# Performance work log

Measured on AMD Instinct MI355X. Metric: run time of the kernel, lower is better.

Reference implementation:

```python
import jax, jax.numpy as jnp
import numpy as np

B, S, D = 1, 2048, 1024          # batch, seq, n_embd
E, F = 16, 1024                  # n_routed_experts, moe_intermediate_size
NG, TKG, K = 4, 2, 4             # n_group, topk_group, num_experts_per_tok
NSH = 2                          # n_shared_experts
SCALE = 2.5                      # routed_scaling_factor
STD = 0.02
EPG = E // NG                    # experts per group


def setup_inputs() -> dict:
    key = jax.random.key(0)
    ks = jax.random.split(key, 8)
    return {
        "hidden_states": jax.random.normal(ks[0], (B, S, D), jnp.float32),
        "router_w": jax.random.normal(ks[1], (E, D), jnp.float32) * STD,   # gate.weight
        "bias": jnp.zeros((E,), jnp.float32),                              # e_score_correction_bias
        "gate_w": jax.random.normal(ks[2], (E, D, F), jnp.float32) * STD,  # per-expert gate_proj (transposed)
        "up_w": jax.random.normal(ks[3], (E, D, F), jnp.float32) * STD,    # per-expert up_proj
        "down_w": jax.random.normal(ks[4], (E, F, D), jnp.float32) * STD,  # per-expert down_proj
        "sh_gate_w": jax.random.normal(ks[5], (D, NSH * F), jnp.float32) * STD,
        "sh_up_w": jax.random.normal(ks[6], (D, NSH * F), jnp.float32) * STD,
        "sh_down_w": jax.random.normal(ks[7], (NSH * F, D), jnp.float32) * STD,
    }


def _route(x_flat, router_w, bias):
    # x_flat: [T, D] -> topk_idx [T, K], topk_w [T, K]
    logits = x_flat.astype(jnp.float32) @ router_w.T          # [T, E]
    scores = jax.nn.sigmoid(logits)
    s = scores + bias[None, :]                                # scores_for_choice
    sg = s.reshape(-1, NG, EPG)
    group_score = jax.lax.top_k(sg, 2)[0].sum(-1)             # sum of top-2 per group [T, NG]
    gidx = jax.lax.top_k(group_score, TKG)[1]                 # [T, TKG]
    gmask = jnp.sum(jax.nn.one_hot(gidx, NG, dtype=jnp.float32), axis=1) > 0   # [T, NG]
    emask = jnp.repeat(gmask, EPG, axis=1)                    # [T, E]
    masked = jnp.where(emask, s, -1.0)
    topk_idx = jax.lax.top_k(masked, K)[1]                    # [T, K]
    tw = jnp.take_along_axis(scores, topk_idx, axis=1)        # gather raw sigmoid scores
    tw = tw / (tw.sum(-1, keepdims=True) + 1e-20)             # norm_topk_prob
    tw = tw * SCALE
    return topk_idx, tw


def reference(hidden_states, router_w, bias, gate_w, up_w, down_w,
              sh_gate_w, sh_up_w, sh_down_w):
    x = hidden_states.reshape(-1, D)                          # [T, D]
    topk_idx, tw = _route(x, router_w, bias)
    # combine weights per (token, expert): scatter-add of topk weights
    combine = (jax.nn.one_hot(topk_idx, E, dtype=tw.dtype) * tw[..., None]).sum(1)  # [T, E]
    # per-expert SwiGLU MLPs (dense dispatch, masked combine == index_add semantics)
    h = jnp.einsum('td,edf->etf', x, gate_w)                  # [E, T, F]
    u = jnp.einsum('td,edf->etf', x, up_w)
    y = jnp.einsum('etf,efd->etd', jax.nn.silu(h) * u, down_w)  # [E, T, D]
    routed = jnp.einsum('etd,te->td', y, combine)             # weighted combine
    # shared experts
    sh = (jax.nn.silu(x @ sh_gate_w) * (x @ sh_up_w)) @ sh_down_w
    return (routed + sh).reshape(hidden_states.shape)
```

## Files before the change

### kernel.cpp

```cpp
#include <hip/hip_runtime.h>
#include <cstdint>
#include <cstddef>


#define T_TOK 2048
#define DIM   1024
#define NEXP  16
#define MAXTILES 80
#define SH_TILES 32
#define GRID_Y (MAXTILES + SH_TILES)
#define NBLK (8 * GRID_Y)
#define ABASE_SH 10240

typedef __bf16 bf16x8_t __attribute__((ext_vector_type(8)));
typedef float  f32x4_t  __attribute__((ext_vector_type(4)));
typedef unsigned short ushort8_t __attribute__((ext_vector_type(8)));
typedef unsigned short ushort4_t __attribute__((ext_vector_type(4)));

#define OFF_XB     (0UL)
#define OFF_SHGT   (4UL<<20)
#define OFF_SHUT   (8UL<<20)
#define OFF_GATET  (12UL<<20)
#define OFF_UPT    (44UL<<20)
#define OFF_DOWNT  (76UL<<20)
#define OFF_SHDT   (108UL<<20)
#define OFF_ACT    (112UL<<20)
#define OFF_YSLOT  (140UL<<20)
#define OFF_PART   (0UL)
#define OFF_CTRL   (160UL<<20)
#define CT_OFFSETS  128
#define CT_NTILES   192
#define CT_TILEEXP  256
#define CT_SLOTTOK  4096
#define CT_TKSLOT   49152
#define CT_TOPKIDX  81920
#define CT_TOPKW    114688

__device__ __forceinline__ unsigned short f2bf(float f) {
  __bf16 h = (__bf16)f;
  return __builtin_bit_cast(unsigned short, h);
}
__device__ __forceinline__ float bf2f(unsigned short u) {
  unsigned int v = ((unsigned int)u) << 16;
  return __builtin_bit_cast(float, v);
}
__device__ __forceinline__ void gld16(const void* g, void* l) {
  __builtin_amdgcn_global_load_lds(
      (const __attribute__((address_space(1))) void*)(g),
      (__attribute__((address_space(3))) void*)(l), 16, 0, 0);
}

__device__ __forceinline__ void tbody(const float* __restrict__ src,
                                      unsigned short* __restrict__ dst,
                                      int R, int C) {
  __shared__ unsigned short tile[64 * 68];
  int cT = blockIdx.x * 64, rT = blockIdx.y * 64;
  int t = threadIdx.x;
  int rb = t >> 4, cb = t & 15;
  float f[4][4];
#pragma unroll
  for (int i = 0; i < 4; i++) {
    float4 v = *(const float4*)(src + (long)(rT + 4 * rb + i) * C + cT + 4 * cb);
    f[i][0] = v.x; f[i][1] = v.y; f[i][2] = v.z; f[i][3] = v.w;
  }
#pragma unroll
  for (int j = 0; j < 4; j++) {
    ushort4_t o;
    o[0] = f2bf(f[0][j]); o[1] = f2bf(f[1][j]); o[2] = f2bf(f[2][j]); o[3] = f2bf(f[3][j]);
    int c = 4 * cb + j;
    *(ushort4_t*)&tile[c * 68 + 4 * rb] = o;
  }
  __syncthreads();
#pragma unroll
  for (int p = 0; p < 2; p++) {
    int q = t + 256 * p;
    int c = q >> 3, r0 = (q & 7) * 8;
    ushort4_t lo = *(const ushort4_t*)&tile[c * 68 + r0];
    ushort4_t hi = *(const ushort4_t*)&tile[c * 68 + r0 + 4];
    ushort8_t w8 = {lo[0], lo[1], lo[2], lo[3], hi[0], hi[1], hi[2], hi[3]};
    *(ushort8_t*)(dst + (long)(cT + c) * R + rT + r0) = w8;
  }
}

__global__ void k_transpose(const float* __restrict__ src, unsigned short* __restrict__ dst,
                            int R, int C) {
  long b = blockIdx.z;
  tbody(src + b * (long)R * C, dst + b * (long)R * C, R, C);
}

__global__ void k_transpose3(const float* __restrict__ g, const float* __restrict__ u,
                             const float* __restrict__ d, unsigned short* __restrict__ gT,
                             unsigned short* __restrict__ uT, unsigned short* __restrict__ dT) {
  int z = blockIdx.z;
  int which = z >> 4;
  long b = z & 15;
  const float* s = (which == 0) ? g : (which == 1) ? u : d;
  unsigned short* t = (which == 0) ? gT : (which == 1) ? uT : dT;
  tbody(s + b * 1048576L, t + b * 1048576L, 1024, 1024);
}

__global__ void k_transpose_sh(const float* __restrict__ sg, const float* __restrict__ su,
                               unsigned short* __restrict__ gT, unsigned short* __restrict__ uT) {
  const float* s = blockIdx.z ? su : sg;
  unsigned short* t = blockIdx.z ? uT : gT;
  tbody(s, t, 1024, 2048);
}

__global__ __launch_bounds__(256) void k_router(
    const float* __restrict__ x, const float* __restrict__ rw,
    const float* __restrict__ bias, int* __restrict__ topk_idx,
    float* __restrict__ topk_w, unsigned short* __restrict__ xb) {
  int t = blockIdx.x, tid = threadIdx.x;
  int wv = tid >> 6, lane = tid & 63;
  float4 xv = ((const float4*)(x + (size_t)t * DIM))[tid];
  ushort4_t xo;
  xo[0] = f2bf(xv.x); xo[1] = f2bf(xv.y); xo[2] = f2bf(xv.z); xo[3] = f2bf(xv.w);
  ((ushort4_t*)(xb + (size_t)t * DIM))[tid] = xo;
  float part[NEXP];
#pragma unroll
  for (int e = 0; e < NEXP; e++) {
    float4 wr = ((const float4*)(rw + (size_t)e * DIM))[tid];
    part[e] = xv.x * wr.x + xv.y * wr.y + xv.z * wr.z + xv.w * wr.w;
  }
  __shared__ float wsum_s[4 * NEXP];
#pragma unroll
  for (int e = 0; e < NEXP; e++) {
    float v = part[e];
#pragma unroll
    for (int off = 32; off; off >>= 1) v += __shfl_xor(v, off, 64);
    if (lane == 0) wsum_s[wv * NEXP + e] = v;
  }
  __syncthreads();
  if (tid == 0) {
    float r_sc[NEXP], r_s[NEXP];
#pragma unroll
    for (int e = 0; e < NEXP; e++) {
      float logit = wsum_s[e] + wsum_s[NEXP + e] + wsum_s[2 * NEXP + e] +
                    wsum_s[3 * NEXP + e];
      float sc = 1.f / (1.f + expf(-logit));
      r_sc[e] = sc;
      r_s[e] = sc + bias[e];
    }
    float gs[4];
#pragma unroll
    for (int g = 0; g < 4; g++) {
      float m1 = -1e30f, m2 = -1e30f;
#pragma unroll
      for (int j = 0; j < 4; j++) {
        float v = r_s[g * 4 + j];
        if (v > m1) { m2 = m1; m1 = v; } else if (v > m2) m2 = v;
      }
      gs[g] = m1 + m2;
    }
    int g1 = 0;
    for (int g = 1; g < 4; g++) if (gs[g] > gs[g1]) g1 = g;
    int g2 = -1;
    for (int g = 0; g < 4; g++) { if (g == g1) continue; if (g2 < 0 || gs[g] > gs[g2]) g2 = g; }
    int taken = 0, idx[4];
    float w[4], wsum = 1e-20f;
#pragma unroll
    for (int k = 0; k < 4; k++) {
      float best = -1e30f; int bi = 0;
#pragma unroll
      for (int e2 = 0; e2 < 16; e2++) {
        if (taken & (1 << e2)) continue;
        int g = e2 >> 2;
        float v = (g == g1 || g == g2) ? r_s[e2] : -1.f;
        if (v > best) { best = v; bi = e2; }
      }
      taken |= 1 << bi; idx[k] = bi;
    }
#pragma unroll
    for (int k = 0; k < 4; k++) { w[k] = r_sc[idx[k]]; wsum += w[k]; }
    float sc2 = 2.5f / wsum;
#pragma unroll
    for (int k = 0; k < 4; k++) {
      topk_idx[t * 4 + k] = idx[k];
      topk_w[t * 4 + k] = w[k] * sc2;
    }
  }
}

__global__ __launch_bounds__(256) void k_route_post(
    const int* __restrict__ topk_idx, int* __restrict__ offsets,
    int* __restrict__ tile_expert, int* __restrict__ n_tiles,
    int* __restrict__ slot_token, int* __restrict__ tk_slot) {
  __shared__ int cnt[NEXP][257];
  __shared__ int offs[NEXP], tot[NEXP];
  int tid = threadIdx.x;
  int4 ent[8];
#pragma unroll
  for (int i = 0; i < 8; i++) ent[i] = ((const int4*)topk_idx)[tid * 8 + i];
  int lc[NEXP];
#pragma unroll
  for (int j = 0; j < NEXP; j++) lc[j] = 0;
#pragma unroll
  for (int i = 0; i < 8; i++) {
    int es[4] = {ent[i].x, ent[i].y, ent[i].z, ent[i].w};
#pragma unroll
    for (int k = 0; k < 4; k++)
#pragma unroll
      for (int j = 0; j < NEXP; j++) lc[j] += (es[k] == j) ? 1 : 0;
  }
#pragma unroll
  for (int j = 0; j < NEXP; j++) cnt[j][tid] = lc[j];
  __syncthreads();
  if (tid < NEXP) {
    int base = 0;
    for (int c = 0; c < 256; c += 8) {
      int v[8];
#pragma unroll
      for (int i = 0; i < 8; i++) v[i] = cnt[tid][c + i];
#pragma unroll
      for (int i = 0; i < 8; i++) { cnt[tid][c + i] = base; base += v[i]; }
    }
    tot[tid] = base;
  }
  __syncthreads();
  if (tid == 0) {
    int cum = 0, tt = 0;
    for (int e = 0; e < NEXP; e++) {
      offs[e] = cum;
      offsets[e] = cum;
      int nt = (tot[e] + 127) >> 7;
      for (int i = 0; i < nt; i++) tile_expert[tt++] = e;
      cum += nt << 7;
    }
    n_tiles[0] = tt;
  }
  __syncthreads();
  for (int e = 0; e < NEXP; e++) {
    int s0 = offs[e] + tot[e];
    int s1 = offs[e] + (((tot[e] + 127) >> 7) << 7);
    for (int s = s0 + tid; s < s1; s += 256) slot_token[s] = -1;
  }
  int lcur[NEXP];
#pragma unroll
  for (int j = 0; j < NEXP; j++) lcur[j] = offs[j] + cnt[j][tid];
#pragma unroll
  for (int i = 0; i < 8; i++) {
    int t = tid * 8 + i;
    int es[4] = {ent[i].x, ent[i].y, ent[i].z, ent[i].w};
#pragma unroll
    for (int k = 0; k < 4; k++) {
      int e = es[k], pos = 0;
#pragma unroll
      for (int j = 0; j < NEXP; j++) pos += (e == j) ? lcur[j] : 0;
#pragma unroll
      for (int j = 0; j < NEXP; j++) lcur[j] += (e == j) ? 1 : 0;
      slot_token[pos] = t;
      tk_slot[t * 4 + k] = pos;
    }
  }
}

__global__ __launch_bounds__(256, 2) void k_gateup(
    const unsigned short* __restrict__ xb, const unsigned short* __restrict__ gateT,
    const unsigned short* __restrict__ upT, const unsigned short* __restrict__ shGT,
    const unsigned short* __restrict__ shUT, unsigned short* __restrict__ act,
    const int* __restrict__ slot_token, const int* __restrict__ tile_expert,
    const int* __restrict__ n_tiles) {
  int o = blockIdx.x;
  int wk = (o & 7) * GRID_Y + (o >> 3);
  int nx = wk & 7, bt = wk >> 3;
  int NT = n_tiles[0];
  bool routed = bt < NT;
  const unsigned short *Bg, *Bu;
  int actbase, tokbase = 0;
  if (routed) {
    int e = tile_expert[bt];
    Bg = gateT + ((size_t)e << 20);
    Bu = upT + ((size_t)e << 20);
    actbase = bt * 128;
  } else {
    int st = bt - NT;
    if (st >= SH_TILES) return;
    int se = st >> 4, tt = st & 15;
    Bg = shGT + ((size_t)se << 20);
    Bu = shUT + ((size_t)se << 20);
    actbase = ABASE_SH + se * T_TOK + tt * 128;
    tokbase = tt * 128;
  }
  int n0 = nx * 128;

  __shared__ unsigned short lds[2 * 3 * 128 * 32];

  int tid = threadIdx.x;
  int w = tid >> 6, L = tid & 63;
  int c0 = w * 128 + L, c1 = c0 + 64;
  int ar0 = c0 >> 2, ar1 = c1 >> 2;
  int ch0 = (c0 & 3) ^ (ar0 & 3), ch1 = (c1 & 3) ^ (ar1 & 3);
  long arow0, arow1;
  if (routed) {
    int t0 = slot_token[bt * 128 + ar0]; if (t0 < 0) t0 = 0;
    int t1 = slot_token[bt * 128 + ar1]; if (t1 < 0) t1 = 0;
    arow0 = t0; arow1 = t1;
  } else {
    arow0 = tokbase + ar0; arow1 = tokbase + ar1;
  }
  const char* aA = (const char*)(xb + arow0 * 1024) + ch0 * 16;
  const char* aB = (const char*)(xb + arow1 * 1024) + ch1 * 16;
  const char* gA = (const char*)(Bg + (size_t)(n0 + ar0) * 1024) + ch0 * 16;
  const char* gB = (const char*)(Bg + (size_t)(n0 + ar1) * 1024) + ch1 * 16;
  const char* uA = (const char*)(Bu + (size_t)(n0 + ar0) * 1024) + ch0 * 16;
  const char* uB = (const char*)(Bu + (size_t)(n0 + ar1) * 1024) + ch1 * 16;
  const int a0o = w * 2048, a1o = w * 2048 + 1024;
  const int g0o = 8192 + w * 2048, g1o = 8192 + w * 2048 + 1024;
  const int u0o = 16384 + w * 2048, u1o = 16384 + w * 2048 + 1024;

  f32x4_t accg[4][4], accu[4][4];
#pragma unroll
  for (int i = 0; i < 4; i++)
#pragma unroll
    for (int j = 0; j < 4; j++) {
      accg[i][j] = f32x4_t{0.f, 0.f, 0.f, 0.f};
      accu[i][j] = f32x4_t{0.f, 0.f, 0.f, 0.f};
    }

  int mb = (w >> 1) * 64, nb = (w & 1) * 64;
  int lr = L & 15, quad = L >> 4;
  int sw = ((quad ^ (lr & 3)) << 3);

#define GU_STAGE(BOFF)                                                       \
  { char* bp = (char*)lds + (BOFF);                                          \
    gld16(aA, bp + a0o); gld16(aB, bp + a1o);                                \
    gld16(gA, bp + g0o); gld16(gB, bp + g1o);                                \
    gld16(uA, bp + u0o); gld16(uB, bp + u1o);                                \
    aA += 64; aB += 64; gA += 64; gB += 64; uA += 64; uB += 64; }

#define GU_COMPUTE(UOFF)                                                     \
  { const unsigned short* pA = lds + (UOFF);                                 \
    const unsigned short* pG = pA + 4096;                                    \
    const unsigned short* pU = pA + 8192;                                    \
    bf16x8_t af[4], bg[4], bu[4];                                            \
    _Pragma("unroll")                                                        \
    for (int i = 0; i < 4; i++) af[i] = *(const bf16x8_t*)(pA + (mb + 16 * i + lr) * 32 + sw); \
    _Pragma("unroll")                                                        \
    for (int i = 0; i < 4; i++) bg[i] = *(const bf16x8_t*)(pG + (nb + 16 * i + lr) * 32 + sw); \
    _Pragma("unroll")                                                        \
    for (int i = 0; i < 4; i++) bu[i] = *(const bf16x8_t*)(pU + (nb + 16 * i + lr) * 32 + sw); \
    _Pragma("unroll")                                                        \
    for (int i = 0; i < 4; i++)                                              \
      _Pragma("unroll")                                                      \
      for (int j = 0; j < 4; j++) {                                          \
        accg[i][j] = __builtin_amdgcn_mfma_f32_16x16x32_bf16(af[i], bg[j], accg[i][j], 0, 0, 0); \
        accu[i][j] = __builtin_amdgcn_mfma_f32_16x16x32_bf16(af[i], bu[j], accu[i][j], 0, 0, 0); \
      } }

  GU_STAGE(0);
  __syncthreads();
#pragma unroll 1
  for (int p = 0; p < 15; ++p) {
    GU_STAGE(24576); GU_COMPUTE(0);     __syncthreads();
    GU_STAGE(0);     GU_COMPUTE(12288); __syncthreads();
  }
  GU_STAGE(24576); GU_COMPUTE(0); __syncthreads();
  GU_COMPUTE(12288);
#undef GU_STAGE
#undef GU_COMPUTE

#pragma unroll
  for (int i = 0; i < 4; i++) {
    int rowb = actbase + mb + 16 * i + quad * 4;
#pragma unroll
    for (int j = 0; j < 4; j++) {
      int col = n0 + nb + 16 * j + lr;
#pragma unroll
      for (int r = 0; r < 4; r++) {
        float h = accg[i][j][r];
        float u = accu[i][j][r];
        float a = h / (1.f + __expf(-h)) * u;
        act[(size_t)(rowb + r) * 1024 + col] = f2bf(a);
      }
    }
  }
}

__global__ __launch_bounds__(256, 2) void k_down(
    const unsigned short* __restrict__ act, const unsigned short* __restrict__ downT,
    const unsigned short* __restrict__ shDT, unsigned short* __restrict__ yslot,
    float* __restrict__ part, const int* __restrict__ tile_expert,
    const int* __restrict__ n_tiles) {
  int o = blockIdx.x;
  int wk = (o & 7) * GRID_Y + (o >> 3);
  int nx = wk & 7, bt = wk >> 3;
  int NT = n_tiles[0];
  bool routed = bt < NT;
  const unsigned short* B;
  size_t bstride;
  int abase, obase, se = 0;
  if (routed) {
    int e = tile_expert[bt];
    B = downT + ((size_t)e << 20);
    bstride = 1024;
    abase = bt * 128;
    obase = bt * 128;
  } else {
    int st = bt - NT;
    if (st >= SH_TILES) return;
    se = st >> 4;
    int tt = st & 15;
    B = shDT + se * 1024;
    bstride = 2048;
    abase = ABASE_SH + se * T_TOK + tt * 128;
    obase = tt * 128;
  }
  int n0 = nx * 128;

  __shared__ unsigned short lds[2 * 2 * 128 * 32];

  int tid = threadIdx.x;
  int w = tid >> 6, L = tid & 63;
  int c0 = w * 128 + L, c1 = c0 + 64;
  int ar0 = c0 >> 2, ar1 = c1 >> 2;
  int ch0 = (c0 & 3) ^ (ar0 & 3), ch1 = (c1 & 3) ^ (ar1 & 3);
  const char* aA = (const char*)(act + (size_t)(abase + ar0) * 1024) + ch0 * 16;
  const char* aB = (const char*)(act + (size_t)(abase + ar1) * 1024) + ch1 * 16;
  const char* bA = (const char*)(B + (size_t)(n0 + ar0) * bstride) + ch0 * 16;
  const char* bB = (const char*)(B + (size_t)(n0 + ar1) * bstride) + ch1 * 16;
  const int a0o = w * 2048, a1o = w * 2048 + 1024;
  const int b0o = 8192 + w * 2048, b1o = 8192 + w * 2048 + 1024;

  f32x4_t acc[4][4];
#pragma unroll
  for (int i = 0; i < 4; i++)
#pragma unroll
    for (int j = 0; j < 4; j++) acc[i][j] = f32x4_t{0.f, 0.f, 0.f, 0.f};

  int mb = (w >> 1) * 64, nb = (w & 1) * 64;
  int lr = L & 15, quad = L >> 4;
  int sw = ((quad ^ (lr & 3)) << 3);

#define DN_STAGE(BOFF)                                                       \
  { char* bp = (char*)lds + (BOFF);                                          \
    gld16(aA, bp + a0o); gld16(aB, bp + a1o);                                \
    gld16(bA, bp + b0o); gld16(bB, bp + b1o);                                \
    aA += 64; aB += 64; bA += 64; bB += 64; }

#define DN_COMPUTE(UOFF)                                                     \
  { const unsigned short* pA = lds + (UOFF);                                 \
    const unsigned short* pB = pA + 4096;                                    \
    bf16x8_t af[4], bb[4];                                                   \
    _Pragma("unroll")                                                        \
    for (int i = 0; i < 4; i++) af[i] = *(const bf16x8_t*)(pA + (mb + 16 * i + lr) * 32 + sw); \
    _Pragma("unroll")                                                        \
    for (int i = 0; i < 4; i++) bb[i] = *(const bf16x8_t*)(pB + (nb + 16 * i + lr) * 32 + sw); \
    _Pragma("unroll")                                                        \
    for (int i = 0; i < 4; i++)                                              \
      _Pragma("unroll")                                                      \
      for (int j = 0; j < 4; j++)                                            \
        acc[i][j] = __builtin_amdgcn_mfma_f32_16x16x32_bf16(af[i], bb[j], acc[i][j], 0, 0, 0); }

  DN_STAGE(0);
  __syncthreads();
#pragma unroll 1
  for (int p = 0; p < 15; ++p) {
    DN_STAGE(16384); DN_COMPUTE(0);    __syncthreads();
    DN_STAGE(0);     DN_COMPUTE(8192); __syncthreads();
  }
  DN_STAGE(16384); DN_COMPUTE(0); __syncthreads();
  DN_COMPUTE(8192);
#undef DN_STAGE
#undef DN_COMPUTE

#pragma unroll
  for (int i = 0; i < 4; i++) {
    int rowb = obase + mb + 16 * i + quad * 4;
#pragma unroll
    for (int j = 0; j < 4; j++) {
      int col = n0 + nb + 16 * j + lr;
#pragma unroll
      for (int r = 0; r < 4; r++) {
        float v = acc[i][j][r];
        if (routed) yslot[(size_t)(rowb + r) * 1024 + col] = f2bf(v);
        else part[(size_t)se * (T_TOK * 1024) + (size_t)(rowb + r) * 1024 + col] = v;
      }
    }
  }
}

__global__ void k_gather(float* __restrict__ out, const float* __restrict__ partial,
                         const unsigned short* __restrict__ yslot,
                         const int* __restrict__ tk_slot, const float* __restrict__ topk_w) {
  int t = blockIdx.x, tid = threadIdx.x;
  int4 sl = ((const int4*)tk_slot)[t];
  float4 wv = ((const float4*)topk_w)[t];
  int d = 4 * tid;
  float4 p0 = *(const float4*)(partial + (size_t)t * 1024 + d);
  float4 p1 = *(const float4*)(partial + (size_t)(T_TOK * 1024) + (size_t)t * 1024 + d);
  float4 o = {p0.x + p1.x, p0.y + p1.y, p0.z + p1.z, p0.w + p1.w};
  const int s[4] = {sl.x, sl.y, sl.z, sl.w};
  const float wk[4] = {wv.x, wv.y, wv.z, wv.w};
#pragma unroll
  for (int k = 0; k < 4; k++) {
    ushort4_t y = *(const ushort4_t*)(yslot + (size_t)s[k] * 1024 + d);
    o.x += wk[k] * bf2f(y[0]);
    o.y += wk[k] * bf2f(y[1]);
    o.z += wk[k] * bf2f(y[2]);
    o.w += wk[k] * bf2f(y[3]);
  }
  *(float4*)(out + (size_t)t * 1024 + d) = o;
}

extern "C" void kernel_launch(void* const* d_in, const int* in_sizes, int n_in,
                              void* d_out, int out_size, void* d_ws, size_t ws_size,
                              hipStream_t stream) {
  const float* x = (const float*)d_in[0];
  const float* rw = (const float*)d_in[1];
  const float* bias = (const float*)d_in[2];
  const float* gw = (const float*)d_in[3];
  const float* uw = (const float*)d_in[4];
  const float* dw = (const float*)d_in[5];
  const float* sg = (const float*)d_in[6];
  const float* su = (const float*)d_in[7];
  const float* sd = (const float*)d_in[8];
  float* out = (float*)d_out;
  char* ws = (char*)d_ws;

  unsigned short* xb    = (unsigned short*)(ws + OFF_XB);
  unsigned short* shGT  = (unsigned short*)(ws + OFF_SHGT);
  unsigned short* shUT  = (unsigned short*)(ws + OFF_SHUT);
  unsigned short* gateT = (unsigned short*)(ws + OFF_GATET);
  unsigned short* upT   = (unsigned short*)(ws + OFF_UPT);
  unsigned short* downT = (unsigned short*)(ws + OFF_DOWNT);
  unsigned short* shDT  = (unsigned short*)(ws + OFF_SHDT);
  unsigned short* act   = (unsigned short*)(ws + OFF_ACT);
  unsigned short* yslot = (unsigned short*)(ws + OFF_YSLOT);
  float*          part  = (float*)(ws + OFF_PART);
  char* ctrl = ws + OFF_CTRL;
  int* offsets_    = (int*)(ctrl + CT_OFFSETS);
  int* n_tiles     = (int*)(ctrl + CT_NTILES);
  int* tile_expert = (int*)(ctrl + CT_TILEEXP);
  int* slot_token  = (int*)(ctrl + CT_SLOTTOK);
  int* tk_slot     = (int*)(ctrl + CT_TKSLOT);
  int* topk_idx    = (int*)(ctrl + CT_TOPKIDX);
  float* topk_w    = (float*)(ctrl + CT_TOPKW);

  k_transpose3<<<dim3(16, 16, 48), 256, 0, stream>>>(gw, uw, dw, gateT, upT, downT);
  k_transpose_sh<<<dim3(32, 16, 2), 256, 0, stream>>>(sg, su, shGT, shUT);
  k_transpose<<<dim3(16, 32, 1), 256, 0, stream>>>(sd, shDT, 2048, 1024);
  k_router<<<2048, 256, 0, stream>>>(x, rw, bias, topk_idx, topk_w, xb);
  k_route_post<<<1, 256, 0, stream>>>(topk_idx, offsets_, tile_expert, n_tiles,
                                      slot_token, tk_slot);
  k_gateup<<<NBLK, 256, 0, stream>>>(xb, gateT, upT, shGT, shUT, act,
                                     slot_token, tile_expert, n_tiles);
  k_down<<<NBLK, 256, 0, stream>>>(act, downT, shDT, yslot, part,
                                   tile_expert, n_tiles);
  k_gather<<<2048, 256, 0, stream>>>(out, part, yslot, tk_slot, topk_w);
}
```

Baseline: 418.0 us.

## Deepen GEMM prefetch with explicit vmcnt waits and enlarge transpose tiles

The gate/up and down GEMM main loops now stage two K-slices ahead. They use explicit s_waitcnt vmcnt counts and raw barriers instead of __syncthreads, so global-to-LDS loads for the next buffer stay in flight while the current one is computed. Separately, each transpose block now handles two 64-row tiles, which halves the grid and gives each thread more loads in flight. The hand-written vmcnt counts must exactly match the number of loads issued per stage, otherwise a buffer can be read before its data arrives.

```diff
diff --git a/kernel.cpp b/kernel.cpp
--- a/kernel.cpp
+++ b/kernel.cpp
@@ -50,36 +50,48 @@
       (__attribute__((address_space(3))) void*)(l), 16, 0, 0);
 }
 
+#define VWAIT6 asm volatile("s_waitcnt vmcnt(6)" ::: "memory")
+#define VWAIT4 asm volatile("s_waitcnt vmcnt(4)" ::: "memory")
+#define VWAIT0 asm volatile("s_waitcnt vmcnt(0)" ::: "memory")
+#define BAR { __builtin_amdgcn_s_barrier(); __builtin_amdgcn_sched_barrier(0); }
+
 __device__ __forceinline__ void tbody(const float* __restrict__ src,
                                       unsigned short* __restrict__ dst,
                                       int R, int C) {
-  __shared__ unsigned short tile[64 * 68];
-  int cT = blockIdx.x * 64, rT = blockIdx.y * 64;
+  __shared__ unsigned short tile[2][64 * 68];
+  int cT = blockIdx.x * 64, rT = blockIdx.y * 128;
   int t = threadIdx.x;
   int rb = t >> 4, cb = t & 15;
-  float f[4][4];
-#pragma unroll
-  for (int i = 0; i < 4; i++) {
-    float4 v = *(const float4*)(src + (long)(rT + 4 * rb + i) * C + cT + 4 * cb);
-    f[i][0] = v.x; f[i][1] = v.y; f[i][2] = v.z; f[i][3] = v.w;
-  }
-#pragma unroll
-  for (int j = 0; j < 4; j++) {
-    ushort4_t o;
-    o[0] = f2bf(f[0][j]); o[1] = f2bf(f[1][j]); o[2] = f2bf(f[2][j]); o[3] = f2bf(f[3][j]);
-    int c = 4 * cb + j;
-    *(ushort4_t*)&tile[c * 68 + 4 * rb] = o;
-  }
+  float f[2][4][4];
+#pragma unroll
+  for (int s = 0; s < 2; s++)
+#pragma unroll
+    for (int i = 0; i < 4; i++) {
+      float4 v = *(const float4*)(src + (long)(rT + s * 64 + 4 * rb + i) * C + cT + 4 * cb);
+      f[s][i][0] = v.x; f[s][i][1] = v.y; f[s][i][2] = v.z; f[s][i][3] = v.w;
+    }
+#pragma unroll
+  for (int s = 0; s < 2; s++)
+#pragma unroll
+    for (int j = 0; j < 4; j++) {
+      ushort4_t o;
+      o[0] = f2bf(f[s][0][j]); o[1] = f2bf(f[s][1][j]);
+      o[2] = f2bf(f[s][2][j]); o[3] = f2bf(f[s][3][j]);
+      int c = 4 * cb + j;
+      *(ushort4_t*)&tile[s][c * 68 + 4 * rb] = o;
+    }
   __syncthreads();
 #pragma unroll
-  for (int p = 0; p < 2; p++) {
-    int q = t + 256 * p;
-    int c = q >> 3, r0 = (q & 7) * 8;
-    ushort4_t lo = *(const ushort4_t*)&tile[c * 68 + r0];
-    ushort4_t hi = *(const ushort4_t*)&tile[c * 68 + r0 + 4];
-    ushort8_t w8 = {lo[0], lo[1], lo[2], lo[3], hi[0], hi[1], hi[2], hi[3]};
-    *(ushort8_t*)(dst + (long)(cT + c) * R + rT + r0) = w8;
-  }
+  for (int s = 0; s < 2; s++)
+#pragma unroll
+    for (int p = 0; p < 2; p++) {
+      int q = t + 256 * p;
+      int c = q >> 3, r0 = (q & 7) * 8;
+      ushort4_t lo = *(const ushort4_t*)&tile[s][c * 68 + r0];
+      ushort4_t hi = *(const ushort4_t*)&tile[s][c * 68 + r0 + 4];
+      ushort8_t w8 = {lo[0], lo[1], lo[2], lo[3], hi[0], hi[1], hi[2], hi[3]};
+      *(ushort8_t*)(dst + (long)(cT + c) * R + rT + s * 64 + r0) = w8;
+    }
 }
 
 __global__ void k_transpose(const float* __restrict__ src, unsigned short* __restrict__ dst,
@@ -347,15 +359,14 @@
         accu[i][j] = __builtin_amdgcn_mfma_f32_16x16x32_bf16(af[i], bu[j], accu[i][j], 0, 0, 0); \
       } }
 
-  GU_STAGE(0);
-  __syncthreads();
+  GU_STAGE(0); GU_STAGE(24576);
 #pragma unroll 1
   for (int p = 0; p < 15; ++p) {
-    GU_STAGE(24576); GU_COMPUTE(0);     __syncthreads();
-    GU_STAGE(0);     GU_COMPUTE(12288); __syncthreads();
-  }
-  GU_STAGE(24576); GU_COMPUTE(0); __syncthreads();
-  GU_COMPUTE(12288);
+    VWAIT6; BAR; GU_COMPUTE(0);     BAR; GU_STAGE(0);
+    VWAIT6; BAR; GU_COMPUTE(12288); BAR; GU_STAGE(24576);
+  }
+  VWAIT6; BAR; GU_COMPUTE(0);
+  VWAIT0; BAR; GU_COMPUTE(12288);
 #undef GU_STAGE
 #undef GU_COMPUTE
 
@@ -451,15 +462,14 @@
       for (int j = 0; j < 4; j++)                                            \
         acc[i][j] = __builtin_amdgcn_mfma_f32_16x16x32_bf16(af[i], bb[j], acc[i][j], 0, 0, 0); }
 
-  DN_STAGE(0);
-  __syncthreads();
+  DN_STAGE(0); DN_STAGE(16384);
 #pragma unroll 1
   for (int p = 0; p < 15; ++p) {
-    DN_STAGE(16384); DN_COMPUTE(0);    __syncthreads();
-    DN_STAGE(0);     DN_COMPUTE(8192); __syncthreads();
-  }
-  DN_STAGE(16384); DN_COMPUTE(0); __syncthreads();
-  DN_COMPUTE(8192);
+    VWAIT4; BAR; DN_COMPUTE(0);    BAR; DN_STAGE(0);
+    VWAIT4; BAR; DN_COMPUTE(8192); BAR; DN_STAGE(16384);
+  }
+  VWAIT4; BAR; DN_COMPUTE(0);
+  VWAIT0; BAR; DN_COMPUTE(8192);
 #undef DN_STAGE
 #undef DN_COMPUTE
 
@@ -536,9 +546,9 @@
   int* topk_idx    = (int*)(ctrl + CT_TOPKIDX);
   float* topk_w    = (float*)(ctrl + CT_TOPKW);
 
-  k_transpose3<<<dim3(16, 16, 48), 256, 0, stream>>>(gw, uw, dw, gateT, upT, downT);
-  k_transpose_sh<<<dim3(32, 16, 2), 256, 0, stream>>>(sg, su, shGT, shUT);
-  k_transpose<<<dim3(16, 32, 1), 256, 0, stream>>>(sd, shDT, 2048, 1024);
+  k_transpose3<<<dim3(16, 8, 48), 256, 0, stream>>>(gw, uw, dw, gateT, upT, downT);
+  k_transpose_sh<<<dim3(32, 8, 2), 256, 0, stream>>>(sg, su, shGT, shUT);
+  k_transpose<<<dim3(16, 16, 1), 256, 0, stream>>>(sd, shDT, 2048, 1024);
   k_router<<<2048, 256, 0, stream>>>(x, rw, bias, topk_idx, topk_w, xb);
   k_route_post<<<1, 256, 0, stream>>>(topk_idx, offsets_, tile_expert, n_tiles,
                                       slot_token, tk_slot);
```

Result: no change. 420.7 us (+0.6%).

## Fuse fp32 weight transpose and bf16 conversion into the GEMM B-tile loads

Applied to the files above, without the earlier changes.

Drops the three separate transpose kernels that converted all expert and shared weights to transposed bf16 in the workspace. The gate/up and down GEMM kernels now load fp32 weight rows straight into registers, convert them to bf16 and write them transposed, with a new swizzle, into LDS, one stage ahead of the compute. This removes a full read of the fp32 weights plus the write and reread of the bf16 copies. In exchange each GEMM reads twice as many weight bytes and spends VALU work and register-staged LDS writes on conversion, and weights for experts that get no tokens are never touched.

```diff
diff --git a/kernel.cpp b/kernel.cpp
--- a/kernel.cpp
+++ b/kernel.cpp
@@ -18,15 +18,9 @@
 typedef unsigned short ushort4_t __attribute__((ext_vector_type(4)));
 
 #define OFF_XB     (0UL)
-#define OFF_SHGT   (4UL<<20)
-#define OFF_SHUT   (8UL<<20)
-#define OFF_GATET  (12UL<<20)
-#define OFF_UPT    (44UL<<20)
-#define OFF_DOWNT  (76UL<<20)
-#define OFF_SHDT   (108UL<<20)
+#define OFF_PART   (16UL<<20)
 #define OFF_ACT    (112UL<<20)
 #define OFF_YSLOT  (140UL<<20)
-#define OFF_PART   (0UL)
 #define OFF_CTRL   (160UL<<20)
 #define CT_OFFSETS  128
 #define CT_NTILES   192
@@ -48,62 +42,6 @@
   __builtin_amdgcn_global_load_lds(
       (const __attribute__((address_space(1))) void*)(g),
       (__attribute__((address_space(3))) void*)(l), 16, 0, 0);
-}
-
-__device__ __forceinline__ void tbody(const float* __restrict__ src,
-                                      unsigned short* __restrict__ dst,
-                                      int R, int C) {
-  __shared__ unsigned short tile[64 * 68];
-  int cT = blockIdx.x * 64, rT = blockIdx.y * 64;
-  int t = threadIdx.x;
-  int rb = t >> 4, cb = t & 15;
-  float f[4][4];
-#pragma unroll
-  for (int i = 0; i < 4; i++) {
-    float4 v = *(const float4*)(src + (long)(rT + 4 * rb + i) * C + cT + 4 * cb);
-    f[i][0] = v.x; f[i][1] = v.y; f[i][2] = v.z; f[i][3] = v.w;
-  }
-#pragma unroll
-  for (int j = 0; j < 4; j++) {
-    ushort4_t o;
-    o[0] = f2bf(f[0][j]); o[1] = f2bf(f[1][j]); o[2] = f2bf(f[2][j]); o[3] = f2bf(f[3][j]);
-    int c = 4 * cb + j;
-    *(ushort4_t*)&tile[c * 68 + 4 * rb] = o;
-  }
-  __syncthreads();
-#pragma unroll
-  for (int p = 0; p < 2; p++) {
-    int q = t + 256 * p;
-    int c = q >> 3, r0 = (q & 7) * 8;
-    ushort4_t lo = *(const ushort4_t*)&tile[c * 68 + r0];
-    ushort4_t hi = *(const ushort4_t*)&tile[c * 68 + r0 + 4];
-    ushort8_t w8 = {lo[0], lo[1], lo[2], lo[3], hi[0], hi[1], hi[2], hi[3]};
-    *(ushort8_t*)(dst + (long)(cT + c) * R + rT + r0) = w8;
-  }
-}
-
-__global__ void k_transpose(const float* __restrict__ src, unsigned short* __restrict__ dst,
-                            int R, int C) {
-  long b = blockIdx.z;
-  tbody(src + b * (long)R * C, dst + b * (long)R * C, R, C);
-}
-
-__global__ void k_transpose3(const float* __restrict__ g, const float* __restrict__ u,
-                             const float* __restrict__ d, unsigned short* __restrict__ gT,
-                             unsigned short* __restrict__ uT, unsigned short* __restrict__ dT) {
-  int z = blockIdx.z;
-  int which = z >> 4;
-  long b = z & 15;
-  const float* s = (which == 0) ? g : (which == 1) ? u : d;
-  unsigned short* t = (which == 0) ? gT : (which == 1) ? uT : dT;
-  tbody(s + b * 1048576L, t + b * 1048576L, 1024, 1024);
-}
-
-__global__ void k_transpose_sh(const float* __restrict__ sg, const float* __restrict__ su,
-                               unsigned short* __restrict__ gT, unsigned short* __restrict__ uT) {
-  const float* s = blockIdx.z ? su : sg;
-  unsigned short* t = blockIdx.z ? uT : gT;
-  tbody(s, t, 1024, 2048);
 }
 
 __global__ __launch_bounds__(256) void k_router(
@@ -255,9 +193,9 @@
 }
 
 __global__ __launch_bounds__(256, 2) void k_gateup(
-    const unsigned short* __restrict__ xb, const unsigned short* __restrict__ gateT,
-    const unsigned short* __restrict__ upT, const unsigned short* __restrict__ shGT,
-    const unsigned short* __restrict__ shUT, unsigned short* __restrict__ act,
+    const unsigned short* __restrict__ xb, const float* __restrict__ gw,
+    const float* __restrict__ uw, const float* __restrict__ sg,
+    const float* __restrict__ su, unsigned short* __restrict__ act,
     const int* __restrict__ slot_token, const int* __restrict__ tile_expert,
     const int* __restrict__ n_tiles) {
   int o = blockIdx.x;
@@ -265,25 +203,28 @@
   int nx = wk & 7, bt = wk >> 3;
   int NT = n_tiles[0];
   bool routed = bt < NT;
-  const unsigned short *Bg, *Bu;
+  const float *Bg, *Bu;
+  size_t sN;
   int actbase, tokbase = 0;
   if (routed) {
     int e = tile_expert[bt];
-    Bg = gateT + ((size_t)e << 20);
-    Bu = upT + ((size_t)e << 20);
+    Bg = gw + ((size_t)e << 20);
+    Bu = uw + ((size_t)e << 20);
+    sN = 1024;
     actbase = bt * 128;
   } else {
     int st = bt - NT;
     if (st >= SH_TILES) return;
     int se = st >> 4, tt = st & 15;
-    Bg = shGT + ((size_t)se << 20);
-    Bu = shUT + ((size_t)se << 20);
+    Bg = sg + se * 1024;
+    Bu = su + se * 1024;
+    sN = 2048;
     actbase = ABASE_SH + se * T_TOK + tt * 128;
     tokbase = tt * 128;
   }
   int n0 = nx * 128;
 
-  __shared__ unsigned short lds[2 * 3 * 128 * 32];
+  __shared__ unsigned short lds[2 * 12288];
 
   int tid = threadIdx.x;
   int w = tid >> 6, L = tid & 63;
@@ -300,13 +241,13 @@
   }
   const char* aA = (const char*)(xb + arow0 * 1024) + ch0 * 16;
   const char* aB = (const char*)(xb + arow1 * 1024) + ch1 * 16;
-  const char* gA = (const char*)(Bg + (size_t)(n0 + ar0) * 1024) + ch0 * 16;
-  const char* gB = (const char*)(Bg + (size_t)(n0 + ar1) * 1024) + ch1 * 16;
-  const char* uA = (const char*)(Bu + (size_t)(n0 + ar0) * 1024) + ch0 * 16;
-  const char* uB = (const char*)(Bu + (size_t)(n0 + ar1) * 1024) + ch1 * 16;
   const int a0o = w * 2048, a1o = w * 2048 + 1024;
-  const int g0o = 8192 + w * 2048, g1o = 8192 + w * 2048 + 1024;
-  const int u0o = 16384 + w * 2048, u1o = 16384 + w * 2048 + 1024;
+
+  int g_ = tid >> 5, m_ = tid & 31;
+  size_t sN4 = sN * 4;
+  const char* pg_ = (const char*)(Bg + (size_t)(4 * g_) * sN + n0 + 4 * m_);
+  const char* pu_ = (const char*)(Bu + (size_t)(4 * g_) * sN + n0 + 4 * m_);
+  float4 rg[4], ru[4];
 
   f32x4_t accg[4][4], accu[4][4];
 #pragma unroll
@@ -319,26 +260,49 @@
 
   int mb = (w >> 1) * 64, nb = (w & 1) * 64;
   int lr = L & 15, quad = L >> 4;
-  int sw = ((quad ^ (lr & 3)) << 3);
-
-#define GU_STAGE(BOFF)                                                       \
-  { char* bp = (char*)lds + (BOFF);                                          \
+  int swA = ((quad ^ (lr & 3)) << 3);
+  int swB = ((quad ^ (lr & 3) ^ ((lr >> 2) & 3)) << 3);
+
+#define GU_BLOAD {                                                           \
+    rg[0] = *(const float4*)(pg_);           rg[1] = *(const float4*)(pg_ + sN4); \
+    rg[2] = *(const float4*)(pg_ + 2 * sN4); rg[3] = *(const float4*)(pg_ + 3 * sN4); \
+    ru[0] = *(const float4*)(pu_);           ru[1] = *(const float4*)(pu_ + sN4); \
+    ru[2] = *(const float4*)(pu_ + 2 * sN4); ru[3] = *(const float4*)(pu_ + 3 * sN4); \
+    pg_ += 32 * sN4; pu_ += 32 * sN4; }
+
+#define GU_AG(BOFF) {                                                        \
+    char* bp = (char*)lds + (BOFF);                                          \
     gld16(aA, bp + a0o); gld16(aB, bp + a1o);                                \
-    gld16(gA, bp + g0o); gld16(gB, bp + g1o);                                \
-    gld16(uA, bp + u0o); gld16(uB, bp + u1o);                                \
-    aA += 64; aB += 64; gA += 64; gB += 64; uA += 64; uB += 64; }
-
-#define GU_COMPUTE(UOFF)                                                     \
-  { const unsigned short* pA = lds + (UOFF);                                 \
+    aA += 64; aB += 64; }
+
+#define GU_BWRITE(BOFF) {                                                    \
+    char* bgp = (char*)lds + (BOFF) + 8192;                                  \
+    char* bup = (char*)lds + (BOFF) + 16384;                                 \
+    _Pragma("unroll")                                                        \
+    for (int j = 0; j < 4; j++) {                                            \
+      int row = 4 * m_ + j;                                                  \
+      int slot = (g_ >> 1) ^ j ^ (m_ & 3);                                   \
+      int off = row * 64 + slot * 16 + (g_ & 1) * 8;                         \
+      ushort4_t pgv, puv;                                                    \
+      pgv[0] = f2bf(rg[0][j]); pgv[1] = f2bf(rg[1][j]);                      \
+      pgv[2] = f2bf(rg[2][j]); pgv[3] = f2bf(rg[3][j]);                      \
+      puv[0] = f2bf(ru[0][j]); puv[1] = f2bf(ru[1][j]);                      \
+      puv[2] = f2bf(ru[2][j]); puv[3] = f2bf(ru[3][j]);                      \
+      *(ushort4_t*)(bgp + off) = pgv;                                        \
+      *(ushort4_t*)(bup + off) = puv;                                        \
+    } }
+
+#define GU_COMPUTE(UOFF) {                                                   \
+    const unsigned short* pA = lds + (UOFF);                                 \
     const unsigned short* pG = pA + 4096;                                    \
     const unsigned short* pU = pA + 8192;                                    \
     bf16x8_t af[4], bg[4], bu[4];                                            \
     _Pragma("unroll")                                                        \
-    for (int i = 0; i < 4; i++) af[i] = *(const bf16x8_t*)(pA + (mb + 16 * i + lr) * 32 + sw); \
-    _Pragma("unroll")                                                        \
-    for (int i = 0; i < 4; i++) bg[i] = *(const bf16x8_t*)(pG + (nb + 16 * i + lr) * 32 + sw); \
-    _Pragma("unroll")                                                        \
-    for (int i = 0; i < 4; i++) bu[i] = *(const bf16x8_t*)(pU + (nb + 16 * i + lr) * 32 + sw); \
+    for (int i = 0; i < 4; i++) af[i] = *(const bf16x8_t*)(pA + (mb + 16 * i + lr) * 32 + swA); \
+    _Pragma("unroll")                                                        \
+    for (int i = 0; i < 4; i++) bg[i] = *(const bf16x8_t*)(pG + (nb + 16 * i + lr) * 32 + swB); \
+    _Pragma("unroll")                                                        \
+    for (int i = 0; i < 4; i++) bu[i] = *(const bf16x8_t*)(pU + (nb + 16 * i + lr) * 32 + swB); \
     _Pragma("unroll")                                                        \
     for (int i = 0; i < 4; i++)                                              \
       _Pragma("unroll")                                                      \
@@ -347,16 +311,25 @@
         accu[i][j] = __builtin_amdgcn_mfma_f32_16x16x32_bf16(af[i], bu[j], accu[i][j], 0, 0, 0); \
       } }
 
-  GU_STAGE(0);
+  GU_BLOAD;
+  GU_BWRITE(0);
+  GU_AG(0);
+  GU_BLOAD;
   __syncthreads();
 #pragma unroll 1
-  for (int p = 0; p < 15; ++p) {
-    GU_STAGE(24576); GU_COMPUTE(0);     __syncthreads();
-    GU_STAGE(0);     GU_COMPUTE(12288); __syncthreads();
-  }
-  GU_STAGE(24576); GU_COMPUTE(0); __syncthreads();
-  GU_COMPUTE(12288);
-#undef GU_STAGE
+  for (int t = 0; t < 32; ++t) {
+    int cur = t & 1;
+    if (t < 31) {
+      GU_BWRITE(cur ? 0 : 24576);
+      GU_AG(cur ? 0 : 24576);
+      if (t < 30) GU_BLOAD;
+    }
+    GU_COMPUTE(cur ? 12288 : 0);
+    __syncthreads();
+  }
+#undef GU_BLOAD
+#undef GU_AG
+#undef GU_BWRITE
 #undef GU_COMPUTE
 
 #pragma unroll
@@ -377,8 +350,8 @@
 }
 
 __global__ __launch_bounds__(256, 2) void k_down(
-    const unsigned short* __restrict__ act, const unsigned short* __restrict__ downT,
-    const unsigned short* __restrict__ shDT, unsigned short* __restrict__ yslot,
+    const unsigned short* __restrict__ act, const float* __restrict__ dw,
+    const float* __restrict__ sd, unsigned short* __restrict__ yslot,
     float* __restrict__ part, const int* __restrict__ tile_expert,
     const int* __restrict__ n_tiles) {
   int o = blockIdx.x;
@@ -386,13 +359,11 @@
   int nx = wk & 7, bt = wk >> 3;
   int NT = n_tiles[0];
   bool routed = bt < NT;
-  const unsigned short* B;
-  size_t bstride;
+  const float* B;
   int abase, obase, se = 0;
   if (routed) {
     int e = tile_expert[bt];
-    B = downT + ((size_t)e << 20);
-    bstride = 1024;
+    B = dw + ((size_t)e << 20);
     abase = bt * 128;
     obase = bt * 128;
   } else {
@@ -400,14 +371,14 @@
     if (st >= SH_TILES) return;
     se = st >> 4;
     int tt = st & 15;
-    B = shDT + se * 1024;
-    bstride = 2048;
+    B = sd + (size_t)se * 1024 * 1024;
     abase = ABASE_SH + se * T_TOK + tt * 128;
     obase = tt * 128;
   }
+  const size_t sN = 1024;
   int n0 = nx * 128;
 
-  __shared__ unsigned short lds[2 * 2 * 128 * 32];
+  __shared__ unsigned short lds[2 * 8192];
 
   int tid = threadIdx.x;
   int w = tid >> 6, L = tid & 63;
@@ -416,10 +387,12 @@
   int ch0 = (c0 & 3) ^ (ar0 & 3), ch1 = (c1 & 3) ^ (ar1 & 3);
   const char* aA = (const char*)(act + (size_t)(abase + ar0) * 1024) + ch0 * 16;
   const char* aB = (const char*)(act + (size_t)(abase + ar1) * 1024) + ch1 * 16;
-  const char* bA = (const char*)(B + (size_t)(n0 + ar0) * bstride) + ch0 * 16;
-  const char* bB = (const char*)(B + (size_t)(n0 + ar1) * bstride) + ch1 * 16;
   const int a0o = w * 2048, a1o = w * 2048 + 1024;
-  const int b0o = 8192 + w * 2048, b1o = 8192 + w * 2048 + 1024;
+
+  int g_ = tid >> 5, m_ = tid & 31;
+  const size_t sN4 = sN * 4;
+  const char* pb_ = (const char*)(B + (size_t)(4 * g_) * sN + n0 + 4 * m_);
+  float4 rb[4];
 
   f32x4_t acc[4][4];
 #pragma unroll
@@ -429,38 +402,65 @@
 
   int mb = (w >> 1) * 64, nb = (w & 1) * 64;
   int lr = L & 15, quad = L >> 4;
-  int sw = ((quad ^ (lr & 3)) << 3);
-
-#define DN_STAGE(BOFF)                                                       \
-  { char* bp = (char*)lds + (BOFF);                                          \
+  int swA = ((quad ^ (lr & 3)) << 3);
+  int swB = ((quad ^ (lr & 3) ^ ((lr >> 2) & 3)) << 3);
+
+#define DN_BLOAD {                                                           \
+    rb[0] = *(const float4*)(pb_);           rb[1] = *(const float4*)(pb_ + sN4); \
+    rb[2] = *(const float4*)(pb_ + 2 * sN4); rb[3] = *(const float4*)(pb_ + 3 * sN4); \
+    pb_ += 32 * sN4; }
+
+#define DN_AG(BOFF) {                                                        \
+    char* bp = (char*)lds + (BOFF);                                          \
     gld16(aA, bp + a0o); gld16(aB, bp + a1o);                                \
-    gld16(bA, bp + b0o); gld16(bB, bp + b1o);                                \
-    aA += 64; aB += 64; bA += 64; bB += 64; }
-
-#define DN_COMPUTE(UOFF)                                                     \
-  { const unsigned short* pA = lds + (UOFF);                                 \
+    aA += 64; aB += 64; }
+
+#define DN_BWRITE(BOFF) {                                                    \
+    char* bbp = (char*)lds + (BOFF) + 8192;                                  \
+    _Pragma("unroll")                                                        \
+    for (int j = 0; j < 4; j++) {                                            \
+      int row = 4 * m_ + j;                                                  \
+      int slot = (g_ >> 1) ^ j ^ (m_ & 3);                                   \
+      int off = row * 64 + slot * 16 + (g_ & 1) * 8;                         \
+      ushort4_t pv;                                                          \
+      pv[0] = f2bf(rb[0][j]); pv[1] = f2bf(rb[1][j]);                        \
+      pv[2] = f2bf(rb[2][j]); pv[3] = f2bf(rb[3][j]);                        \
+      *(ushort4_t*)(bbp + off) = pv;                                         \
+    } }
+
+#define DN_COMPUTE(UOFF) {                                                   \
+    const unsigned short* pA = lds + (UOFF);                                 \
     const unsigned short* pB = pA + 4096;                                    \
     bf16x8_t af[4], bb[4];                                                   \
     _Pragma("unroll")                                                        \
-    for (int i = 0; i < 4; i++) af[i] = *(const bf16x8_t*)(pA + (mb + 16 * i + lr) * 32 + sw); \
-    _Pragma("unroll")                                                        \
-    for (int i = 0; i < 4; i++) bb[i] = *(const bf16x8_t*)(pB + (nb + 16 * i + lr) * 32 + sw); \
+    for (int i = 0; i < 4; i++) af[i] = *(const bf16x8_t*)(pA + (mb + 16 * i + lr) * 32 + swA); \
+    _Pragma("unroll")                                                        \
+    for (int i = 0; i < 4; i++) bb[i] = *(const bf16x8_t*)(pB + (nb + 16 * i + lr) * 32 + swB); \
     _Pragma("unroll")                                                        \
     for (int i = 0; i < 4; i++)                                              \
       _Pragma("unroll")                                                      \
       for (int j = 0; j < 4; j++)                                            \
         acc[i][j] = __builtin_amdgcn_mfma_f32_16x16x32_bf16(af[i], bb[j], acc[i][j], 0, 0, 0); }
 
-  DN_STAGE(0);
+  DN_BLOAD;
+  DN_BWRITE(0);
+  DN_AG(0);
+  DN_BLOAD;
   __syncthreads();
 #pragma unroll 1
-  for (int p = 0; p < 15; ++p) {
-    DN_STAGE(16384); DN_COMPUTE(0);    __syncthreads();
-    DN_STAGE(0);     DN_COMPUTE(8192); __syncthreads();
-  }
-  DN_STAGE(16384); DN_COMPUTE(0); __syncthreads();
-  DN_COMPUTE(8192);
-#undef DN_STAGE
+  for (int t = 0; t < 32; ++t) {
+    int cur = t & 1;
+    if (t < 31) {
+      DN_BWRITE(cur ? 0 : 16384);
+      DN_AG(cur ? 0 : 16384);
+      if (t < 30) DN_BLOAD;
+    }
+    DN_COMPUTE(cur ? 8192 : 0);
+    __syncthreads();
+  }
+#undef DN_BLOAD
+#undef DN_AG
+#undef DN_BWRITE
 #undef DN_COMPUTE
 
 #pragma unroll
@@ -518,12 +518,6 @@
   char* ws = (char*)d_ws;
 
   unsigned short* xb    = (unsigned short*)(ws + OFF_XB);
-  unsigned short* shGT  = (unsigned short*)(ws + OFF_SHGT);
-  unsigned short* shUT  = (unsigned short*)(ws + OFF_SHUT);
-  unsigned short* gateT = (unsigned short*)(ws + OFF_GATET);
-  unsigned short* upT   = (unsigned short*)(ws + OFF_UPT);
-  unsigned short* downT = (unsigned short*)(ws + OFF_DOWNT);
-  unsigned short* shDT  = (unsigned short*)(ws + OFF_SHDT);
   unsigned short* act   = (unsigned short*)(ws + OFF_ACT);
   unsigned short* yslot = (unsigned short*)(ws + OFF_YSLOT);
   float*          part  = (float*)(ws + OFF_PART);
@@ -536,15 +530,12 @@
   int* topk_idx    = (int*)(ctrl + CT_TOPKIDX);
   float* topk_w    = (float*)(ctrl + CT_TOPKW);
 
-  k_transpose3<<<dim3(16, 16, 48), 256, 0, stream>>>(gw, uw, dw, gateT, upT, downT);
-  k_transpose_sh<<<dim3(32, 16, 2), 256, 0, stream>>>(sg, su, shGT, shUT);
-  k_transpose<<<dim3(16, 32, 1), 256, 0, stream>>>(sd, shDT, 2048, 1024);
   k_router<<<2048, 256, 0, stream>>>(x, rw, bias, topk_idx, topk_w, xb);
   k_route_post<<<1, 256, 0, stream>>>(topk_idx, offsets_, tile_expert, n_tiles,
                                       slot_token, tk_slot);
-  k_gateup<<<NBLK, 256, 0, stream>>>(xb, gateT, upT, shGT, shUT, act,
+  k_gateup<<<NBLK, 256, 0, stream>>>(xb, gw, uw, sg, su, act,
                                      slot_token, tile_expert, n_tiles);
-  k_down<<<NBLK, 256, 0, stream>>>(act, downT, shDT, yslot, part,
+  k_down<<<NBLK, 256, 0, stream>>>(act, dw, sd, yslot, part,
                                    tile_expert, n_tiles);
   k_gather<<<2048, 256, 0, stream>>>(out, part, yslot, tk_slot, topk_w);
 }
```

New measurement: 406.7 us. -2.7%, faster.
